# Optimization experiments

Hardware: AMD Instinct MI355X
Metric: run time of the kernel (lower is better)

Reference implementation:

```python
import jax, jax.numpy as jnp
import numpy as np

# Module constants (from init_kwargs)
NOISE_NUM = 64
SAMPLE_NUM = 262144
FCL = 65                 # filter_coeff_length
FL = 64                  # frame_length
GAIN = 1.0               # attenuate_gain
FRAME_NUM = SAMPLE_NUM // FL + 1   # 4097
IR = 2 * FCL - 1         # 129, linear-phase IR length
CONV = IR + FL - 1       # 192, per-frame filtered length
LOG10 = float(np.log(10.0))


def modified_sigmoid(x):
    # DDSP modified sigmoid: 2*sigmoid(x)^log(10) + 1e-7
    return 2.0 * jax.nn.sigmoid(x) ** LOG10 + 1e-7


def setup_inputs() -> dict:
    key = jax.random.key(0)
    k1, k2 = jax.random.split(key)
    coefficient_bank = jax.random.uniform(k1, (NOISE_NUM, FRAME_NUM, FCL),
                                          dtype=jnp.float32, minval=-1.0, maxval=1.0)
    noise = jax.random.uniform(k2, (NOISE_NUM, FRAME_NUM, FL), dtype=jnp.float32)
    return {"coefficient_bank": coefficient_bank, "noise": noise}


def reference(coefficient_bank, noise):
    B, F, L = coefficient_bank.shape  # (64, 4097, 65)
    # Zero-phase frequency response -> impulse response
    fr = modified_sigmoid(coefficient_bank)                  # (B,F,L) real half-spectrum
    zp_ir = jnp.fft.irfft(fr, n=IR, axis=-1)                 # (B,F,129)
    lp_ir = jnp.roll(zp_ir, L - 1, axis=-1)                  # linear phase
    # periodic hann window of length IR (torch.hann_window periodic=True)
    win = 0.5 * (1.0 - jnp.cos(2.0 * jnp.pi * jnp.arange(IR, dtype=jnp.float32) / IR))
    wir = lp_ir * win
    # FFT-domain filtering of per-frame noise (linear convolution length CONV)
    H = jnp.fft.rfft(jnp.pad(wir, ((0, 0), (0, 0), (0, FL - 1))), axis=-1)   # (B,F,97)
    n = noise * 2.0 - 1.0                                                    # uniform [-1,1)
    N = jnp.fft.rfft(jnp.pad(n, ((0, 0), (0, 0), (0, IR - 1))), axis=-1)     # (B,F,97)
    filtered = jnp.fft.irfft(N * H, n=CONV, axis=-1) * GAIN                  # (B,F,192)
    # Overlap-add with hop FL (replaces conv_transpose1d with identity kernel)
    total = (F - 1) * FL + CONV
    idx = (jnp.arange(F)[:, None] * FL + jnp.arange(CONV)[None, :]).reshape(-1)
    out = jnp.zeros((B, total), dtype=filtered.dtype).at[:, idx].add(filtered.reshape(B, -1))
    return out[:, :SAMPLE_NUM]
```

## Files before the change

kernel.cpp:

```cpp
#include <hip/hip_runtime.h>


#define NB 64
#define FTOT 4097
#define FCL 65
#define SAMPLES 262144
#define OUT_FRAMES 4096
#define G 32
#define NF (G + 2)
#define PW 196
#define BLOCKS_PER_B (OUT_FRAMES / G)

__device__ __forceinline__ float mod_sigmoid(float x) {
    float s = 1.0f / (1.0f + __expf(-x));
    return 2.0f * __expf(2.302585092994046f * __logf(s)) + 1e-7f;
}

__device__ __forceinline__ float rdlane(float v, int k) {
    return __int_as_float(__builtin_amdgcn_readlane(__float_as_int(v), k));
}

__device__ __forceinline__ void conv_dd(const float4* __restrict__ wb,
                                        const float4* __restrict__ np4,
                                        int S0, int S1, float a[8]) {
    float4 W1 = wb[16 - S0];
    float4 W2 = wb[17 - S0];
    #pragma unroll 4
    for (int s4 = S0; s4 < S1; ++s4) {
        float4 W0 = wb[15 - s4];
        float4 u  = np4[s4];
        float nv[4] = {__builtin_fmaf(u.x, 2.f, -1.f),
                       __builtin_fmaf(u.y, 2.f, -1.f),
                       __builtin_fmaf(u.z, 2.f, -1.f),
                       __builtin_fmaf(u.w, 2.f, -1.f)};
        float w[12] = {W0.x, W0.y, W0.z, W0.w,
                       W1.x, W1.y, W1.z, W1.w,
                       W2.x, W2.y, W2.z, W2.w};
        #pragma unroll
        for (int i = 0; i < 4; ++i)
            #pragma unroll
            for (int j = 0; j < 8; ++j)
                a[j] = __builtin_fmaf(nv[i], w[4 + j - i], a[j]);
        W2 = W1; W1 = W0;
    }
}

__global__ __launch_bounds__(256, 5) void fn_kernel(
    const float* __restrict__ coeff,
    const float* __restrict__ noise,
    float* __restrict__ out)
{
    __shared__ __align__(16) float wirP[NF * PW];

    const int tid  = threadIdx.x;
    const int lane = tid & 63;
    const int wv   = tid >> 6;
    const int blk  = blockIdx.x;
    const int b    = blk / BLOCKS_PER_B;
    const int cg   = blk % BLOCKS_PER_B;
    const int fp0  = cg * G;
    const int fbase = fp0 - 2;

    for (int i = tid; i < NF * 18; i += 256) {
        int row = i / 18, z = i - row * 18;
        int qz = (z < 9) ? z : (z + 31);
        ((float4*)wirP)[row * 49 + qz] = make_float4(0.f, 0.f, 0.f, 0.f);
    }

    float frv[9], f64v[9], vm[9];
    #pragma unroll
    for (int i = 0; i < 9; ++i) {
        int fi = wv + 4 * i;
        int f  = fbase + fi;
        vm[i] = (f >= 0 && fi < NF) ? 1.f : 0.f;
        int fl = f < 0 ? 0 : (f > FTOT - 1 ? FTOT - 1 : f);
        const float* row = coeff + ((size_t)b * FTOT + fl) * FCL;
        frv[i]  = row[lane];
        f64v[i] = row[64];
    }
    #pragma unroll
    for (int i = 0; i < 9; ++i) {
        frv[i]  = mod_sigmoid(frv[i]);
        f64v[i] = mod_sigmoid(f64v[i]);
    }

    __syncthreads();

    {
        float c  = __cosf(6.283185307179586f * (float)lane * (1.0f / 129.0f));
        float c2 = 2.0f * c;
        float cp = 1.0f;
        float ck = c;
        float S[9];
        #pragma unroll
        for (int i = 0; i < 9; ++i) S[i] = 0.5f * rdlane(frv[i], 0);
        #pragma unroll 8
        for (int k = 1; k < 64; ++k) {
            #pragma unroll
            for (int i = 0; i < 9; ++i)
                S[i] = __builtin_fmaf(rdlane(frv[i], k), ck, S[i]);
            float cn = __builtin_fmaf(c2, ck, -cp);
            cp = ck; ck = cn;
        }
        #pragma unroll
        for (int i = 0; i < 9; ++i)
            S[i] = __builtin_fmaf(f64v[i], ck, S[i]);
        float w1f = 0.5f - 0.5f * __cosf(6.283185307179586f * (float)(64 + lane) * (1.0f / 129.0f));
        float w2f = 0.5f - 0.5f * __cosf(6.283185307179586f * (float)(64 - lane) * (1.0f / 129.0f));
        #pragma unroll
        for (int i = 0; i < 9; ++i) {
            int fi = wv + 4 * i;
            if (fi < NF) {
                float zp = S[i] * (2.0f / 129.0f) * vm[i];
                wirP[fi * PW + 96 + lane] = w1f * zp;
                wirP[fi * PW + 96 - lane] = w2f * zp;
            }
        }
    }
    __syncthreads();

    {
        const int chunk = tid & 31;
        const int t     = tid >> 5;
        float a[8];
        #pragma unroll
        for (int j = 0; j < 8; ++j) a[j] = 0.0f;

        #pragma unroll
        for (int dd = 0; dd < 3; ++dd) {
            const int q  = chunk + 2 - dd;
            const int fq = fbase + q;
            const int fc = fq < 0 ? 0 : fq;
            const float4* np4 = (const float4*)(noise + ((size_t)b * FTOT + fc) * 64);
            const float4* wb  = (const float4*)wirP + q * 49 + (16 * dd + 2 * t - 8);
            int S0 = (dd == 2) ? 4 * wv : 0;
            int S1 = (dd == 0) ? 4 * wv + 4 : 16;
            conv_dd(wb, np4, S0, S1, a);
        }

        float* op = &out[(size_t)b * SAMPLES + (size_t)(fp0 + chunk) * 64 + t * 8];
        *(float4*)op       = make_float4(a[0], a[1], a[2], a[3]);
        *(float4*)(op + 4) = make_float4(a[4], a[5], a[6], a[7]);
    }
}

extern "C" void kernel_launch(void* const* d_in, const int* in_sizes, int n_in,
                              void* d_out, int out_size, void* d_ws, size_t ws_size,
                              hipStream_t stream) {
    const float* coeff = (const float*)d_in[0];
    const float* noise = (const float*)d_in[1];
    float* out = (float*)d_out;
    dim3 grid(NB * BLOCKS_PER_B);
    fn_kernel<<<grid, 256, 0, stream>>>(coeff, noise, out);
}
```

Measured before the change: 301.1 us.

## Double frames per block, stage sigmoid spectra in LDS, widen per-thread conv tile

```diff
diff --git a/kernel.cpp b/kernel.cpp
--- a/kernel.cpp
+++ b/kernel.cpp
@@ -6,9 +6,10 @@
 #define FCL 65
 #define SAMPLES 262144
 #define OUT_FRAMES 4096
-#define G 32
+#define G 64
 #define NF (G + 2)
 #define PW 196
+#define NFR 17
 #define BLOCKS_PER_B (OUT_FRAMES / G)
 
 __device__ __forceinline__ float mod_sigmoid(float x) {
@@ -16,15 +17,13 @@
     return 2.0f * __expf(2.302585092994046f * __logf(s)) + 1e-7f;
 }
 
-__device__ __forceinline__ float rdlane(float v, int k) {
-    return __int_as_float(__builtin_amdgcn_readlane(__float_as_int(v), k));
-}
-
 __device__ __forceinline__ void conv_dd(const float4* __restrict__ wb,
                                         const float4* __restrict__ np4,
-                                        int S0, int S1, float a[8]) {
+                                        int S0, int S1, float a[16]) {
     float4 W1 = wb[16 - S0];
     float4 W2 = wb[17 - S0];
+    float4 W3 = wb[18 - S0];
+    float4 W4 = wb[19 - S0];
     #pragma unroll 4
     for (int s4 = S0; s4 < S1; ++s4) {
         float4 W0 = wb[15 - s4];
@@ -33,19 +32,21 @@
                        __builtin_fmaf(u.y, 2.f, -1.f),
                        __builtin_fmaf(u.z, 2.f, -1.f),
                        __builtin_fmaf(u.w, 2.f, -1.f)};
-        float w[12] = {W0.x, W0.y, W0.z, W0.w,
+        float w[20] = {W0.x, W0.y, W0.z, W0.w,
                        W1.x, W1.y, W1.z, W1.w,
-                       W2.x, W2.y, W2.z, W2.w};
+                       W2.x, W2.y, W2.z, W2.w,
+                       W3.x, W3.y, W3.z, W3.w,
+                       W4.x, W4.y, W4.z, W4.w};
         #pragma unroll
         for (int i = 0; i < 4; ++i)
             #pragma unroll
-            for (int j = 0; j < 8; ++j)
+            for (int j = 0; j < 16; ++j)
                 a[j] = __builtin_fmaf(nv[i], w[4 + j - i], a[j]);
-        W2 = W1; W1 = W0;
+        W4 = W3; W3 = W2; W2 = W1; W1 = W0;
     }
 }
 
-__global__ __launch_bounds__(256, 5) void fn_kernel(
+__global__ __launch_bounds__(256, 3) void fn_kernel(
     const float* __restrict__ coeff,
     const float* __restrict__ noise,
     float* __restrict__ out)
@@ -61,54 +62,75 @@
     const int fp0  = cg * G;
     const int fbase = fp0 - 2;
 
-    for (int i = tid; i < NF * 18; i += 256) {
-        int row = i / 18, z = i - row * 18;
-        int qz = (z < 9) ? z : (z + 31);
-        ((float4*)wirP)[row * 49 + qz] = make_float4(0.f, 0.f, 0.f, 0.f);
+    for (int r = tid; r < NF; r += 256)
+        wirP[r * PW + 32] = 0.f;
+
+    {
+        const int frsoff = (lane < 32) ? (160 + lane) : (lane - 32);
+        #pragma unroll
+        for (int i = 0; i < NFR; ++i) {
+            int fi = wv + 4 * i;
+            if (fi < NF) {
+                int f  = fbase + fi;
+                int fc = f < 0 ? 0 : f;
+                float u = coeff[((size_t)b * FTOT + fc) * FCL + lane];
+                wirP[fi * PW + frsoff] = mod_sigmoid(u);
+            }
+        }
+        if (tid < NF) {
+            int f  = fbase + tid;
+            int fc = f < 0 ? 0 : f;
+            wirP[tid * PW + 192] = mod_sigmoid(coeff[((size_t)b * FTOT + fc) * FCL + 64]);
+        }
     }
-
-    float frv[9], f64v[9], vm[9];
-    #pragma unroll
-    for (int i = 0; i < 9; ++i) {
-        int fi = wv + 4 * i;
-        int f  = fbase + fi;
-        vm[i] = (f >= 0 && fi < NF) ? 1.f : 0.f;
-        int fl = f < 0 ? 0 : (f > FTOT - 1 ? FTOT - 1 : f);
-        const float* row = coeff + ((size_t)b * FTOT + fl) * FCL;
-        frv[i]  = row[lane];
-        f64v[i] = row[64];
-    }
-    #pragma unroll
-    for (int i = 0; i < 9; ++i) {
-        frv[i]  = mod_sigmoid(frv[i]);
-        f64v[i] = mod_sigmoid(f64v[i]);
-    }
-
     __syncthreads();
 
     {
+        int rofs[NFR];
+        float vm[NFR];
+        #pragma unroll
+        for (int i = 0; i < NFR; ++i) {
+            int fi  = wv + 4 * i;
+            vm[i]   = (fbase + fi >= 0) ? 1.f : 0.f;
+            int fic = fi < NF ? fi : (NF - 1);
+            rofs[i] = fic * PW;
+        }
         float c  = __cosf(6.283185307179586f * (float)lane * (1.0f / 129.0f));
         float c2 = 2.0f * c;
         float cp = 1.0f;
         float ck = c;
-        float S[9];
+        float S[NFR];
         #pragma unroll
-        for (int i = 0; i < 9; ++i) S[i] = 0.5f * rdlane(frv[i], 0);
-        #pragma unroll 8
-        for (int k = 1; k < 64; ++k) {
+        for (int k4 = 0; k4 < 16; ++k4) {
+            const int off = (k4 < 8) ? (160 + 4 * k4) : (4 * (k4 - 8));
+            float4 V[NFR];
             #pragma unroll
-            for (int i = 0; i < 9; ++i)
-                S[i] = __builtin_fmaf(rdlane(frv[i], k), ck, S[i]);
-            float cn = __builtin_fmaf(c2, ck, -cp);
-            cp = ck; ck = cn;
+            for (int i = 0; i < NFR; ++i)
+                V[i] = *(const float4*)&wirP[rofs[i] + off];
+            #pragma unroll
+            for (int kk = 0; kk < 4; ++kk) {
+                if (k4 == 0 && kk == 0) {
+                    #pragma unroll
+                    for (int i = 0; i < NFR; ++i) S[i] = 0.5f * V[i].x;
+                } else {
+                    #pragma unroll
+                    for (int i = 0; i < NFR; ++i) {
+                        float vk = (kk == 0) ? V[i].x : (kk == 1) ? V[i].y
+                                 : (kk == 2) ? V[i].z : V[i].w;
+                        S[i] = __builtin_fmaf(vk, ck, S[i]);
+                    }
+                    float cn = __builtin_fmaf(c2, ck, -cp);
+                    cp = ck; ck = cn;
+                }
+            }
         }
         #pragma unroll
-        for (int i = 0; i < 9; ++i)
-            S[i] = __builtin_fmaf(f64v[i], ck, S[i]);
+        for (int i = 0; i < NFR; ++i)
+            S[i] = __builtin_fmaf(wirP[rofs[i] + 192], ck, S[i]);
         float w1f = 0.5f - 0.5f * __cosf(6.283185307179586f * (float)(64 + lane) * (1.0f / 129.0f));
         float w2f = 0.5f - 0.5f * __cosf(6.283185307179586f * (float)(64 - lane) * (1.0f / 129.0f));
         #pragma unroll
-        for (int i = 0; i < 9; ++i) {
+        for (int i = 0; i < NFR; ++i) {
             int fi = wv + 4 * i;
             if (fi < NF) {
                 float zp = S[i] * (2.0f / 129.0f) * vm[i];
@@ -119,12 +141,19 @@
     }
     __syncthreads();
 
+    for (int idx = tid; idx < NF * 17; idx += 256) {
+        int r = idx / 17, z = idx - r * 17;
+        int q = (z < 8) ? z : (z + 32);
+        *(float4*)&wirP[r * PW + 4 * q] = make_float4(0.f, 0.f, 0.f, 0.f);
+    }
+    __syncthreads();
+
     {
-        const int chunk = tid & 31;
-        const int t     = tid >> 5;
-        float a[8];
+        const int chunk = tid & 63;
+        const int t     = tid >> 6;
+        float a[16];
         #pragma unroll
-        for (int j = 0; j < 8; ++j) a[j] = 0.0f;
+        for (int j = 0; j < 16; ++j) a[j] = 0.0f;
 
         #pragma unroll
         for (int dd = 0; dd < 3; ++dd) {
@@ -132,15 +161,17 @@
             const int fq = fbase + q;
             const int fc = fq < 0 ? 0 : fq;
             const float4* np4 = (const float4*)(noise + ((size_t)b * FTOT + fc) * 64);
-            const float4* wb  = (const float4*)wirP + q * 49 + (16 * dd + 2 * t - 8);
-            int S0 = (dd == 2) ? 4 * wv : 0;
-            int S1 = (dd == 0) ? 4 * wv + 4 : 16;
+            const float4* wb  = (const float4*)wirP + q * 49 + (16 * dd + 4 * t - 8);
+            int S0 = (dd == 2) ? 4 * t : 0;
+            int S1 = (dd == 0) ? 4 * t + 4 : 16;
             conv_dd(wb, np4, S0, S1, a);
         }
 
-        float* op = &out[(size_t)b * SAMPLES + (size_t)(fp0 + chunk) * 64 + t * 8];
-        *(float4*)op       = make_float4(a[0], a[1], a[2], a[3]);
-        *(float4*)(op + 4) = make_float4(a[4], a[5], a[6], a[7]);
+        float* op = &out[(size_t)b * SAMPLES + (size_t)(fp0 + chunk) * 64 + t * 16];
+        *(float4*)op        = make_float4(a[0],  a[1],  a[2],  a[3]);
+        *(float4*)(op + 4)  = make_float4(a[4],  a[5],  a[6],  a[7]);
+        *(float4*)(op + 8)  = make_float4(a[8],  a[9],  a[10], a[11]);
+        *(float4*)(op + 12) = make_float4(a[12], a[13], a[14], a[15]);
     }
 }
 
```

New measurement: 521.8 us. 73.3% more time.
